# Optimization experiments

Hardware: AMD Instinct MI355X
Metric: run time of the kernel (lower is better)

Reference implementation:

```python
import jax, jax.numpy as jnp
import numpy as np

COST_CLASS, COST_MASK, COST_DICE = 2.0, 5.0, 5.0
NUM_POINTS = 12544

def setup_inputs() -> dict:
    key = jax.random.key(0)
    k1, k2, k3, k4, k5 = jax.random.split(key, 5)
    bs, Q, K = 4, 100, 134
    H = W = 256
    M = 80
    P = H * W
    pred_logits = jax.random.normal(k1, (bs, Q, K), dtype=jnp.float32)
    pred_masks = jax.random.normal(k2, (bs, Q, H, W), dtype=jnp.float32)
    tgt_labels = jax.random.randint(k3, (M,), 0, K - 1, dtype=jnp.int32)
    # binary target masks, stored as float (matches .float() in torch code)
    tgt_masks = (jax.random.uniform(k4, (M, H, W)) > 0.5).astype(jnp.float32)
    # random subset of points without replacement (torch.randperm[:num_points])
    point_idx = jax.random.permutation(k5, P)[:NUM_POINTS].astype(jnp.int32)
    return {"pred_logits": pred_logits, "pred_masks": pred_masks,
            "tgt_labels": tgt_labels, "tgt_masks": tgt_masks,
            "point_idx": point_idx}

def reference(pred_logits, pred_masks, tgt_labels, tgt_masks, point_idx):
    bs, Q, K = pred_logits.shape
    N = bs * Q
    M = tgt_masks.shape[0]
    Pn = point_idx.shape[0]

    # class cost: -p[n, tgt_id[m]]
    out_prob = jax.nn.softmax(pred_logits.reshape(N, K), axis=-1)
    tgt_ids = jnp.clip(tgt_labels.astype(jnp.int32), 0, K - 1)
    cost_class = -out_prob[:, tgt_ids]                      # (N, M)

    # sampled mask logits / targets
    x = pred_masks.reshape(N, -1)[:, point_idx]             # (N, Pn) logits
    y = tgt_masks.reshape(M, -1)[:, point_idx]              # (M, Pn) binary float

    # BCE-with-logits cost, separable form:
    # mean_p[softplus(x) - x*y] = mean_p softplus(x) - (x @ y^T)/Pn
    sp_mean = jnp.mean(jax.nn.softplus(x), axis=-1)         # (N,)
    xy = jnp.einsum('np,mp->nm', x, y)                      # (N, M)
    cost_mask = sp_mean[:, None] - xy / Pn

    # dice cost
    s = jax.nn.sigmoid(x)                                   # (N, Pn)
    numer = 2.0 * jnp.einsum('np,mp->nm', s, y)             # (N, M)
    denom = jnp.sum(s, axis=-1)[:, None] + jnp.sum(y, axis=-1)[None, :]
    cost_dice = 1.0 - (numer + 1.0) / (denom + 1.0)

    C = COST_CLASS * cost_class + COST_MASK * cost_mask + COST_DICE * cost_dice
    return C.reshape(bs, Q, M)
```

## Files before the change

kernel.cpp:

```cpp
#include <hip/hip_runtime.h>
#include <math.h>

#define N_ROWS 400
#define M_ROWS 80
#define K_CLS  134
#define PN     12544
#define PFULL  65536
#define WORDS  (PFULL / 32)
#define NSUB   25
#define KCG    49
#define NM     (N_ROWS * M_ROWS)
#define CHUNK  8192
#define CWORDS (CHUNK / 32)
#define CPB    (PFULL / CHUNK)
#define SPAN   192

typedef __attribute__((ext_vector_type(4))) float  f32x4;
typedef __attribute__((ext_vector_type(8))) __bf16 bf16x8;

__device__ __forceinline__ float wave_reduce_sum(float v) {
#pragma unroll
    for (int off = 32; off > 0; off >>= 1) v += __shfl_down(v, off, 64);
    return v;
}

__global__ __launch_bounds__(1024) void sort_softmax_kernel(
        const int* __restrict__ point_idx,
        unsigned int* __restrict__ bitmap_g, int* __restrict__ rank_g,
        int* __restrict__ cw_g,
        float* __restrict__ rowS_acc, float* __restrict__ rowSP_acc,
        float* __restrict__ ysum_acc,
        const float* __restrict__ pred_logits,
        float* __restrict__ rowmax, float* __restrict__ rowsum) {
    int tid = threadIdx.x;
    if (blockIdx.x == 0) {
        __shared__ unsigned int bits[WORDS];
        __shared__ int wtot[16], wbase[16];
        bits[tid] = 0u; bits[tid + 1024] = 0u;
        if (tid < N_ROWS) { rowS_acc[tid] = 0.f; rowSP_acc[tid] = 0.f; }
        if (tid < M_ROWS) ysum_acc[tid] = 0.f;
        __syncthreads();
        for (int i = tid; i < PN; i += 1024) {
            int p = point_idx[i];
            atomicOr(&bits[p >> 5], 1u << (p & 31));
        }
        __syncthreads();
        unsigned int w0 = bits[tid * 2], w1 = bits[tid * 2 + 1];
        int c0 = __popc(w0), c1 = __popc(w1);
        int cnt = c0 + c1;
        int lane = tid & 63, wid = tid >> 6;
        int v = cnt;
#pragma unroll
        for (int off = 1; off < 64; off <<= 1) {
            int u = __shfl_up(v, off, 64);
            if (lane >= off) v += u;
        }
        if (lane == 63) wtot[wid] = v;
        __syncthreads();
        if (tid == 0) {
            int run = 0;
#pragma unroll
            for (int i = 0; i < 16; ++i) { wbase[i] = run; run += wtot[i]; }
        }
        __syncthreads();
        int base = wbase[wid] + (v - cnt);
        bitmap_g[tid * 2]     = w0;
        bitmap_g[tid * 2 + 1] = w1;
        rank_g[tid * 2]       = base;
        rank_g[tid * 2 + 1]   = base + c0;
        {
            int rb = base, c = c0, w = tid * 2;
            int kc = (rb + 255) >> 8;
            if (c > 0 && kc < KCG && kc * 256 < rb + c) cw_g[kc] = w;
        }
        {
            int rb = base + c0, c = c1, w = tid * 2 + 1;
            int kc = (rb + 255) >> 8;
            if (c > 0 && kc < KCG && kc * 256 < rb + c) cw_g[kc] = w;
        }
    } else {
        int wave = tid >> 6, lane = tid & 63;
        int n = (blockIdx.x - 1) * 16 + wave;
        const float* row = pred_logits + n * K_CLS;
        float mx = -1e30f;
        for (int k = lane; k < K_CLS; k += 64) mx = fmaxf(mx, row[k]);
#pragma unroll
        for (int off = 32; off > 0; off >>= 1) mx = fmaxf(mx, __shfl_down(mx, off, 64));
        mx = __shfl(mx, 0, 64);
        float se = 0.f;
        for (int k = lane; k < K_CLS; k += 64) se += expf(row[k] - mx);
        se = wave_reduce_sum(se);
        if (lane == 0) { rowmax[n] = mx; rowsum[n] = se; }
    }
}

__global__ __launch_bounds__(256) void buildY_kernel(
        const float* __restrict__ tgt_masks,
        const unsigned int* __restrict__ bitmap_g, const int* __restrict__ rank_g,
        __bf16* __restrict__ Yc, float* __restrict__ ysum_acc) {
    __shared__ __bf16 comp[CHUNK];
    __shared__ unsigned int sb[CWORDS];
    __shared__ int swb[CWORDS];
    __shared__ float a0[4];
    int b   = blockIdx.x;
    int m = b / CPB, ch = b % CPB;
    int tid = threadIdx.x;
    int wave = tid >> 6, lane = tid & 63;
    int w0  = ch * CWORDS;
    int gb  = rank_g[w0];
    int end = (w0 + CWORDS == WORDS) ? PN : rank_g[w0 + CWORDS];
    int cnt = end - gb;
    sb[tid]  = bitmap_g[w0 + tid];
    swb[tid] = rank_g[w0 + tid] - gb;
    __syncthreads();
    const float* src = tgt_masks + (size_t)m * PFULL + ch * CHUNK;
#pragma unroll
    for (int it = 0; it < CHUNK / (256 * 4); ++it) {
        int e = (it * 256 + tid) * 4;
        f32x4 v = *(const f32x4*)(src + e);
        unsigned int w = sb[e >> 5];
        int bp = e & 31;
        int r0 = swb[e >> 5] + __popc(w & ((1u << bp) - 1u));
        unsigned int m4 = (w >> bp) & 0xFu;
        if (m4 & 1u) comp[r0] = (__bf16)((v[0] > 0.5f) ? 1.f : 0.f);
        if (m4 & 2u) comp[r0 + __popc(m4 & 1u)] = (__bf16)((v[1] > 0.5f) ? 1.f : 0.f);
        if (m4 & 4u) comp[r0 + __popc(m4 & 3u)] = (__bf16)((v[2] > 0.5f) ? 1.f : 0.f);
        if (m4 & 8u) comp[r0 + __popc(m4 & 7u)] = (__bf16)((v[3] > 0.5f) ? 1.f : 0.f);
    }
    __syncthreads();
    __bf16* yrow = Yc + (size_t)m * PN + gb;
    float ys = 0.f;
    for (int i = tid; i < cnt; i += 256) {
        __bf16 y = comp[i];
        yrow[i] = y;
        ys += (float)y;
    }
    ys = wave_reduce_sum(ys);
    if (lane == 0) a0[wave] = ys;
    __syncthreads();
    if (tid == 0)
        atomicAdd(&ysum_acc[m], a0[0] + a0[1] + a0[2] + a0[3]);
}

__global__ __launch_bounds__(256) void gemm_fused_kernel(
        const float* __restrict__ pred_masks,
        const __bf16* __restrict__ Yc,
        const unsigned int* __restrict__ bitmap_g,
        const int* __restrict__ rank_g, const int* __restrict__ cw_g,
        float* __restrict__ xypart, float* __restrict__ sypart,
        float* __restrict__ rowS_acc, float* __restrict__ rowSP_acc) {
    __shared__ __bf16 comp[16 * 272];
    __shared__ unsigned int sw[SPAN];
    __shared__ int sr[SPAN];
    __shared__ float red[4][20][64];
    __shared__ float rowred[4][2][16];
    int tid = threadIdx.x;
    int wave = tid >> 6, lane = tid & 63;
    int colL = lane & 15, quad = lane >> 4;
    int nsub = blockIdx.x % NSUB, kcg = blockIdx.x / NSUB;
    int n0 = nsub * 16;
    int wlo = cw_g[kcg];
    int ew  = (kcg == KCG - 1) ? (WORDS - 1) : cw_g[kcg + 1];
    int S = ew - wlo + 1; if (S > SPAN) S = SPAN;
    int rbase = kcg * 256;
    for (int i = tid; i < S; i += 256) {
        sw[i] = bitmap_g[wlo + i];
        sr[i] = rank_g[wlo + i] - rbase;
    }
    bf16x8 Bb[2][5];
#pragma unroll
    for (int i = 0; i < 2; ++i) {
        int k0 = kcg * 256 + (wave * 2 + i) * 32 + quad * 8;
#pragma unroll
        for (int j = 0; j < 5; ++j)
            Bb[i][j] = *(const bf16x8*)(Yc + (size_t)(16 * j + colL) * PN + k0);
    }
    __syncthreads();

    int E4 = S * 8;
#pragma unroll
    for (int rr = 0; rr < 4; ++rr) {
        int row = wave + rr * 4;
        const float* src = pred_masks + (size_t)(n0 + row) * PFULL + (size_t)wlo * 32;
        __bf16* crow = comp + row * 272;
        for (int e4 = lane; e4 < E4; e4 += 64) {
            f32x4 v = *(const f32x4*)(src + e4 * 4);
            unsigned int w = sw[e4 >> 3];
            int bp = (e4 & 7) * 4;
            int r0 = sr[e4 >> 3] + __popc(w & ((1u << bp) - 1u));
            unsigned int m4 = (w >> bp) & 0xFu;
            int r1 = r0 + (int)(m4 & 1u);
            int r2 = r0 + __popc(m4 & 3u);
            int r3 = r0 + __popc(m4 & 7u);
            if ((m4 & 1u) && (unsigned)r0 < 256u) crow[r0] = (__bf16)v[0];
            if ((m4 & 2u) && (unsigned)r1 < 256u) crow[r1] = (__bf16)v[1];
            if ((m4 & 4u) && (unsigned)r2 < 256u) crow[r2] = (__bf16)v[2];
            if ((m4 & 8u) && (unsigned)r3 < 256u) crow[r3] = (__bf16)v[3];
        }
    }
    __syncthreads();

    f32x4 accX[5], accS[5];
    f32x4 zero = {0.f, 0.f, 0.f, 0.f};
#pragma unroll
    for (int j = 0; j < 5; ++j) { accX[j] = zero; accS[j] = zero; }
    float sS = 0.f, sSP = 0.f;
#pragma unroll
    for (int i = 0; i < 2; ++i) {
        int kl = (wave * 2 + i) * 32 + quad * 8;
        bf16x8 aX = *(const bf16x8*)&comp[colL * 272 + kl];
        bf16x8 aSg;
#pragma unroll
        for (int jj = 0; jj < 8; ++jj) {
            float x  = (float)aX[jj];
            float ax = fabsf(x);
            float ee = __expf(-ax);
            float den = 1.f + ee;
            float inv = __builtin_amdgcn_rcpf(den);
            float sig = (x >= 0.f) ? inv : ee * inv;
            float sp  = fmaxf(x, 0.f) + __logf(den);
            aSg[jj] = (__bf16)sig;
            sS += sig; sSP += sp;
        }
#pragma unroll
        for (int j = 0; j < 5; ++j) {
            accX[j] = __builtin_amdgcn_mfma_f32_16x16x32_bf16(aX,  Bb[i][j], accX[j], 0, 0, 0);
            accS[j] = __builtin_amdgcn_mfma_f32_16x16x32_bf16(aSg, Bb[i][j], accS[j], 0, 0, 0);
        }
    }
    sS  += __shfl_down(sS, 32, 64);
    sS  += __shfl_down(sS, 16, 64);
    sSP += __shfl_down(sSP, 32, 64);
    sSP += __shfl_down(sSP, 16, 64);
    if (lane < 16) { rowred[wave][0][lane] = sS; rowred[wave][1][lane] = sSP; }

#pragma unroll
    for (int j = 0; j < 5; ++j)
#pragma unroll
        for (int r = 0; r < 4; ++r) red[wave][j * 4 + r][lane] = accX[j][r];
    __syncthreads();
#pragma unroll
    for (int v0 = 0; v0 < 5; ++v0) {
        int v = wave * 5 + v0;
        float s = red[0][v][lane] + red[1][v][lane] + red[2][v][lane] + red[3][v][lane];
        int j = v >> 2, r = v & 3;
        int n = n0 + quad * 4 + r, m = 16 * j + colL;
        xypart[(size_t)kcg * NM + n * M_ROWS + m] = s;
    }
    if (tid < 16) {
        atomicAdd(&rowS_acc[n0 + tid],
                  rowred[0][0][tid] + rowred[1][0][tid] +
                  rowred[2][0][tid] + rowred[3][0][tid]);
    } else if (tid < 32) {
        int l = tid - 16;
        atomicAdd(&rowSP_acc[n0 + l],
                  rowred[0][1][l] + rowred[1][1][l] +
                  rowred[2][1][l] + rowred[3][1][l]);
    }
    __syncthreads();
#pragma unroll
    for (int j = 0; j < 5; ++j)
#pragma unroll
        for (int r = 0; r < 4; ++r) red[wave][j * 4 + r][lane] = accS[j][r];
    __syncthreads();
#pragma unroll
    for (int v0 = 0; v0 < 5; ++v0) {
        int v = wave * 5 + v0;
        float s = red[0][v][lane] + red[1][v][lane] + red[2][v][lane] + red[3][v][lane];
        int j = v >> 2, r = v & 3;
        int n = n0 + quad * 4 + r, m = 16 * j + colL;
        sypart[(size_t)kcg * NM + n * M_ROWS + m] = s;
    }
}

__global__ __launch_bounds__(256) void combine_kernel(
        const float* __restrict__ logits,
        const int* __restrict__ tgt_labels,
        const float* __restrict__ rowmax,
        const float* __restrict__ rowsum,
        const float* __restrict__ rowS_acc,
        const float* __restrict__ rowSP_acc,
        const float* __restrict__ ysum_acc,
        const float* __restrict__ xypart,
        const float* __restrict__ sypart,
        float* __restrict__ out) {
    __shared__ float sxy[4][64], ssy[4][64];
    int il = threadIdx.x & 63, q = threadIdx.x >> 6;
    int idx = blockIdx.x * 64 + il;
    int n = idx / M_ROWS, m = idx % M_ROWS;
    float xy = 0.f, sy = 0.f;
    for (int g = q; g < KCG; g += 4) {
        xy += xypart[(size_t)g * NM + idx];
        sy += sypart[(size_t)g * NM + idx];
    }
    sxy[q][il] = xy; ssy[q][il] = sy;
    __syncthreads();
    if (q == 0) {
        xy = sxy[0][il] + sxy[1][il] + sxy[2][il] + sxy[3][il];
        sy = ssy[0][il] + ssy[1][il] + ssy[2][il] + ssy[3][il];
        float ss = rowS_acc[n], sp = rowSP_acc[n], ysum = ysum_acc[m];
        int tc = tgt_labels[m];
        tc = min(max(tc, 0), K_CLS - 1);
        float p = expf(logits[n * K_CLS + tc] - rowmax[n]) / rowsum[n];
        float cost_class = -p;
        float cost_mask = (sp - xy) * (1.0f / PN);
        float cost_dice = 1.f - (2.f * sy + 1.f) / (ss + ysum + 1.f);
        out[idx] = 2.f * cost_class + 5.f * cost_mask + 5.f * cost_dice;
    }
}

extern "C" void kernel_launch(void* const* d_in, const int* in_sizes, int n_in,
                              void* d_out, int out_size, void* d_ws, size_t ws_size,
                              hipStream_t stream) {
    const float* pred_logits = (const float*)d_in[0];
    const float* pred_masks  = (const float*)d_in[1];
    const int*   tgt_labels  = (const int*)d_in[2];
    const float* tgt_masks   = (const float*)d_in[3];
    const int*   point_idx   = (const int*)d_in[4];
    float* out = (float*)d_out;

    char* ws = (char*)d_ws;
    size_t off = 0;
    auto carve = [&](size_t nbytes) {
        char* p = ws + off;
        off += (nbytes + 255) & ~(size_t)255;
        return p;
    };
    unsigned int* bitmap = (unsigned int*)carve(WORDS * 4);
    int*   rankp  = (int*)carve(WORDS * 4);
    int*   cw     = (int*)carve(KCG * 4);
    float* rowmax = (float*)carve(N_ROWS * 4);
    float* rowsum = (float*)carve(N_ROWS * 4);
    float* rowS_acc  = (float*)carve(N_ROWS * 4);
    float* rowSP_acc = (float*)carve(N_ROWS * 4);
    float* ysum_acc  = (float*)carve(M_ROWS * 4);
    __bf16* Yc = (__bf16*)carve((size_t)M_ROWS * PN * 2);
    float* xypart = (float*)carve((size_t)KCG * NM * 4);
    float* sypart = (float*)carve((size_t)KCG * NM * 4);
    (void)ws_size; (void)in_sizes; (void)n_in; (void)out_size;

    sort_softmax_kernel<<<26, 1024, 0, stream>>>(
        point_idx, bitmap, rankp, cw, rowS_acc, rowSP_acc, ysum_acc,
        pred_logits, rowmax, rowsum);
    buildY_kernel<<<M_ROWS * CPB, 256, 0, stream>>>(
        tgt_masks, bitmap, rankp, Yc, ysum_acc);
    gemm_fused_kernel<<<NSUB * KCG, 256, 0, stream>>>(
        pred_masks, Yc, bitmap, rankp, cw, xypart, sypart,
        rowS_acc, rowSP_acc);
    combine_kernel<<<NM / 64, 256, 0, stream>>>(
        pred_logits, tgt_labels, rowmax, rowsum, rowS_acc, rowSP_acc,
        ysum_acc, xypart, sypart, out);
}
```

Baseline: 215.7 us.

## Batch gather loads, branchless LDS scatter, and alias shared memory in GEMM kernel

In the fused GEMM kernel, the compaction loop now issues all NIT=8 vector loads of pred_masks up front, then scatters them. Invalid lanes are clamped to a valid address and write to a trash slot in the row padding instead of branching. The shared-memory arrays are packed into one aliased buffer: the reduction buffer reuses the compaction area, protected by an added barrier, and SPAN shrinks from 192 to 64. Together these cut LDS footprint to raise occupancy and give more memory parallelism. The same branchless trash-slot scatter is applied in buildY. The risk is that the fixed 8×64 element coverage and SPAN=64 must hold for every point group.

```diff
diff --git a/kernel.cpp b/kernel.cpp
--- a/kernel.cpp
+++ b/kernel.cpp
@@ -13,7 +13,8 @@
 #define CHUNK  8192
 #define CWORDS (CHUNK / 32)
 #define CPB    (PFULL / CHUNK)
-#define SPAN   192
+#define SPAN   64
+#define NIT    8
 
 typedef __attribute__((ext_vector_type(4))) float  f32x4;
 typedef __attribute__((ext_vector_type(8))) __bf16 bf16x8;
@@ -98,7 +99,7 @@
         const float* __restrict__ tgt_masks,
         const unsigned int* __restrict__ bitmap_g, const int* __restrict__ rank_g,
         __bf16* __restrict__ Yc, float* __restrict__ ysum_acc) {
-    __shared__ __bf16 comp[CHUNK];
+    __shared__ __bf16 comp[CHUNK + 16];
     __shared__ unsigned int sb[CWORDS];
     __shared__ int swb[CWORDS];
     __shared__ float a0[4];
@@ -114,18 +115,23 @@
     swb[tid] = rank_g[w0 + tid] - gb;
     __syncthreads();
     const float* src = tgt_masks + (size_t)m * PFULL + ch * CHUNK;
+    int t = CHUNK + (lane & 15);
 #pragma unroll
     for (int it = 0; it < CHUNK / (256 * 4); ++it) {
         int e = (it * 256 + tid) * 4;
         f32x4 v = *(const f32x4*)(src + e);
         unsigned int w = sb[e >> 5];
         int bp = e & 31;
-        int r0 = swb[e >> 5] + __popc(w & ((1u << bp) - 1u));
+        int rb = swb[e >> 5] + __popc(w & ((1u << bp) - 1u));
         unsigned int m4 = (w >> bp) & 0xFu;
-        if (m4 & 1u) comp[r0] = (__bf16)((v[0] > 0.5f) ? 1.f : 0.f);
-        if (m4 & 2u) comp[r0 + __popc(m4 & 1u)] = (__bf16)((v[1] > 0.5f) ? 1.f : 0.f);
-        if (m4 & 4u) comp[r0 + __popc(m4 & 3u)] = (__bf16)((v[2] > 0.5f) ? 1.f : 0.f);
-        if (m4 & 8u) comp[r0 + __popc(m4 & 7u)] = (__bf16)((v[3] > 0.5f) ? 1.f : 0.f);
+        int r0 = (m4 & 1u) ? rb : t;
+        int r1 = (m4 & 2u) ? rb + (int)(m4 & 1u) : t;
+        int r2 = (m4 & 4u) ? rb + __popc(m4 & 3u) : t;
+        int r3 = (m4 & 8u) ? rb + __popc(m4 & 7u) : t;
+        comp[r0] = (__bf16)((v[0] > 0.5f) ? 1.f : 0.f);
+        comp[r1] = (__bf16)((v[1] > 0.5f) ? 1.f : 0.f);
+        comp[r2] = (__bf16)((v[2] > 0.5f) ? 1.f : 0.f);
+        comp[r3] = (__bf16)((v[3] > 0.5f) ? 1.f : 0.f);
     }
     __syncthreads();
     __bf16* yrow = Yc + (size_t)m * PN + gb;
@@ -149,11 +155,13 @@
         const int* __restrict__ rank_g, const int* __restrict__ cw_g,
         float* __restrict__ xypart, float* __restrict__ sypart,
         float* __restrict__ rowS_acc, float* __restrict__ rowSP_acc) {
-    __shared__ __bf16 comp[16 * 272];
-    __shared__ unsigned int sw[SPAN];
-    __shared__ int sr[SPAN];
-    __shared__ float red[4][20][64];
-    __shared__ float rowred[4][2][16];
+    __shared__ __align__(16) unsigned char smem[20992];
+    __bf16* comp      = (__bf16*)smem;
+    unsigned int* sw  = (unsigned int*)(smem + 8704);
+    int* sr           = (int*)(smem + 8960);
+    float (*red)[20][64] = (float (*)[20][64])smem;
+    float (*rowred)[2][16] = (float (*)[2][16])(smem + 20480);
+
     int tid = threadIdx.x;
     int wave = tid >> 6, lane = tid & 63;
     int colL = lane & 15, quad = lane >> 4;
@@ -162,6 +170,7 @@
     int wlo = cw_g[kcg];
     int ew  = (kcg == KCG - 1) ? (WORDS - 1) : cw_g[kcg + 1];
     int S = ew - wlo + 1; if (S > SPAN) S = SPAN;
+    int E4 = S * 8;
     int rbase = kcg * 256;
     for (int i = tid; i < S; i += 256) {
         sw[i] = bitmap_g[wlo + i];
@@ -177,25 +186,39 @@
     }
     __syncthreads();
 
-    int E4 = S * 8;
-#pragma unroll
+    int trash = 256 + (lane & 15);
+#pragma unroll 1
     for (int rr = 0; rr < 4; ++rr) {
         int row = wave + rr * 4;
         const float* src = pred_masks + (size_t)(n0 + row) * PFULL + (size_t)wlo * 32;
         __bf16* crow = comp + row * 272;
-        for (int e4 = lane; e4 < E4; e4 += 64) {
-            f32x4 v = *(const f32x4*)(src + e4 * 4);
-            unsigned int w = sw[e4 >> 3];
-            int bp = (e4 & 7) * 4;
-            int r0 = sr[e4 >> 3] + __popc(w & ((1u << bp) - 1u));
+        f32x4 vb[NIT];
+#pragma unroll
+        for (int it = 0; it < NIT; ++it) {
+            int e4 = lane + it * 64;
+            int e4c = (e4 < E4) ? e4 : (E4 - 1);
+            vb[it] = *(const f32x4*)(src + (size_t)e4c * 4);
+        }
+#pragma unroll
+        for (int it = 0; it < NIT; ++it) {
+            int e4 = lane + it * 64;
+            int e4c = (e4 < E4) ? e4 : (E4 - 1);
+            unsigned int w = sw[e4c >> 3];
+            int bp = (e4c & 7) * 4;
+            int rb = sr[e4c >> 3] + __popc(w & ((1u << bp) - 1u));
             unsigned int m4 = (w >> bp) & 0xFu;
-            int r1 = r0 + (int)(m4 & 1u);
-            int r2 = r0 + __popc(m4 & 3u);
-            int r3 = r0 + __popc(m4 & 7u);
-            if ((m4 & 1u) && (unsigned)r0 < 256u) crow[r0] = (__bf16)v[0];
-            if ((m4 & 2u) && (unsigned)r1 < 256u) crow[r1] = (__bf16)v[1];
-            if ((m4 & 4u) && (unsigned)r2 < 256u) crow[r2] = (__bf16)v[2];
-            if ((m4 & 8u) && (unsigned)r3 < 256u) crow[r3] = (__bf16)v[3];
+            int r0 = rb;
+            int r1 = rb + (int)(m4 & 1u);
+            int r2 = rb + __popc(m4 & 3u);
+            int r3 = rb + __popc(m4 & 7u);
+            r0 = ((m4 & 1u) && (unsigned)r0 < 256u) ? r0 : trash;
+            r1 = ((m4 & 2u) && (unsigned)r1 < 256u) ? r1 : trash;
+            r2 = ((m4 & 4u) && (unsigned)r2 < 256u) ? r2 : trash;
+            r3 = ((m4 & 8u) && (unsigned)r3 < 256u) ? r3 : trash;
+            crow[r0] = (__bf16)vb[it][0];
+            crow[r1] = (__bf16)vb[it][1];
+            crow[r2] = (__bf16)vb[it][2];
+            crow[r3] = (__bf16)vb[it][3];
         }
     }
     __syncthreads();
@@ -233,6 +256,7 @@
     sSP += __shfl_down(sSP, 32, 64);
     sSP += __shfl_down(sSP, 16, 64);
     if (lane < 16) { rowred[wave][0][lane] = sS; rowred[wave][1][lane] = sSP; }
+    __syncthreads();
 
 #pragma unroll
     for (int j = 0; j < 5; ++j)
```

After: 206.8 us. 4.1% less time.
